# Optimization experiments

Measured on AMD Instinct MI355X. Metric: run time of the kernel, lower is better.

## Reference

```python
import jax, jax.numpy as jnp
import numpy as np

NUM_LEVELS = 16
LEVEL_DIM = 2
BASE_RES = 16
MAX_RES = 2048
HASHMAP_SIZE = 1 << 19
N_POINTS = 2000000

# Instant-NGP geometric progression of grid resolutions
_scale = np.exp2(np.log2(MAX_RES / BASE_RES) / (NUM_LEVELS - 1))
RESOLUTIONS = [int(np.ceil(BASE_RES * _scale ** l)) for l in range(NUM_LEVELS)]

# corner offsets of the unit cube, shape [8, 3]
_OFFS = np.stack(np.meshgrid([0, 1], [0, 1], [0, 1], indexing='ij'), -1).reshape(8, 3)
_PRIMES = np.array([1, 2654435761, 805459861], dtype=np.uint32)


def grid_encode(x, table):
    """x: [N,3] in [0,1]; table: [L, T, F] -> [N, L*F]."""
    offs = jnp.asarray(_OFFS, dtype=jnp.int32)          # [8,3]
    feats = []
    for l, res in enumerate(RESOLUTIONS):
        pos = x * (res - 1)                              # [N,3]
        pos_i = jnp.clip(jnp.floor(pos).astype(jnp.int32), 0, res - 2)
        frac = pos - pos_i.astype(pos.dtype)             # [N,3]
        corners = pos_i[:, None, :] + offs[None]         # [N,8,3]
        if res ** 3 <= HASHMAP_SIZE:
            # dense (collision-free) indexing for coarse levels
            idx = corners[..., 0] + res * (corners[..., 1] + res * corners[..., 2])
        else:
            # spatial hash: xor of coordinate * prime, mod table size
            c = corners.astype(jnp.uint32)
            h = (c[..., 0] * _PRIMES[0]) ^ (c[..., 1] * _PRIMES[1]) ^ (c[..., 2] * _PRIMES[2])
            idx = (h % jnp.uint32(HASHMAP_SIZE)).astype(jnp.int32)
        vals = table[l][idx]                             # [N,8,F] gather
        # multilinear interpolation weights per corner
        w = jnp.prod(jnp.where(offs[None].astype(bool), frac[:, None, :], 1.0 - frac[:, None, :]), axis=-1)  # [N,8]
        feats.append(jnp.einsum('nc,ncf->nf', w, vals))
    return jnp.concatenate(feats, axis=-1)               # [N, 32]


def setup_inputs() -> dict:
    key = jax.random.key(0)
    ks = jax.random.split(key, 6)
    x = jax.random.uniform(ks[0], (N_POINTS, 3), dtype=jnp.float32)
    table = jax.random.uniform(ks[1], (NUM_LEVELS, HASHMAP_SIZE, LEVEL_DIM),
                               dtype=jnp.float32, minval=-1e-4, maxval=1e-4)
    in_dim = NUM_LEVELS * LEVEL_DIM  # 32
    W1 = jax.random.normal(ks[2], (in_dim, 64), dtype=jnp.float32) / np.sqrt(in_dim)
    W2 = jax.random.normal(ks[3], (64, 64), dtype=jnp.float32) / 8.0
    W3 = jax.random.normal(ks[4], (64, 64), dtype=jnp.float32) / 8.0
    Wo = jax.random.normal(ks[5], (64, 1), dtype=jnp.float32) / 8.0
    z = lambda n: jnp.zeros((n,), dtype=jnp.float32)
    return {"x": x, "table": table, "W1": W1, "b1": z(64), "W2": W2, "b2": z(64),
            "W3": W3, "b3": z(64), "Wo": Wo, "bo": z(1)}


def reference(x, table, W1, b1, W2, b2, W3, b3, Wo, bo):
    h = grid_encode(x, table)                 # [N,32]
    h = jax.nn.relu(h @ W1 + b1)
    h = jax.nn.relu(h @ W2 + b2)
    h = jax.nn.relu(h @ W3 + b3)
    return h @ Wo + bo                        # [N,1]
```

## Files before the change

### kernel.cpp

```cpp
#include <hip/hip_runtime.h>
#include <cmath>
#include <cstdint>


#define HASH_SZ (1u << 19)
#define HMASK   (HASH_SZ - 1u)
#define PR2 2654435761u
#define PR3 805459861u

typedef float v2f __attribute__((ext_vector_type(2)));
typedef float v4f __attribute__((ext_vector_type(4)));
typedef v4f v4fu __attribute__((aligned(8)));
typedef v2f v2fu __attribute__((aligned(8)));
typedef short bf16x8 __attribute__((ext_vector_type(8)));
typedef float f32x4 __attribute__((ext_vector_type(4)));
typedef unsigned int u32;
typedef u32 u32x2 __attribute__((ext_vector_type(2)));
typedef u32 u32x4 __attribute__((ext_vector_type(4)));

struct ResArr { int r[16]; };

__device__ __forceinline__ unsigned short bf16_rne(float f) {
    union { float f; unsigned u; } v; v.f = f;
    unsigned u = v.u;
    unsigned r = (u + 0x7fffu + ((u >> 16) & 1u)) >> 16;
    return (unsigned short)r;
}
__device__ __forceinline__ float bf16f(unsigned short h) {
    union { unsigned u; float f; } v; v.u = ((unsigned)h) << 16;
    return v.f;
}
__device__ __forceinline__ void split8(const float* x, bf16x8& hi, bf16x8& lo) {
    #pragma unroll
    for (int j = 0; j < 8; ++j) {
        union { float f; unsigned u; } v; v.f = x[j];
        const unsigned hu = v.u & 0xffff0000u;
        hi[j] = (short)(hu >> 16);
        union { unsigned u; float f; } hf; hf.u = hu;
        const float d = x[j] - hf.f;
        union { float f; unsigned u; } dv; dv.f = d;
        lo[j] = (short)((dv.u + 0x7fffu + ((dv.u >> 16) & 1u)) >> 16);
    }
}
__device__ __forceinline__ u32 rne16u(float f) {
    union { float f; u32 u; } v; v.f = f;
    return (v.u + 0x7fffu + ((v.u >> 16) & 1u)) >> 16;
}
__device__ __forceinline__ u32x2 pack_split2(float f0, float f1) {
    union { float f; u32 u; } a, b; a.f = f0; b.f = f1;
    const u32 h0 = a.u & 0xffff0000u, h1 = b.u & 0xffff0000u;
    union { u32 u; float f; } ha, hb; ha.u = h0; hb.u = h1;
    u32x2 r;
    r.x = (h0 >> 16) | h1;
    r.y = rne16u(f0 - ha.f) | (rne16u(f1 - hb.f) << 16);
    return r;
}

__device__ __forceinline__ void gather_one(
    const v2f* __restrict__ tbl, int res, bool dense,
    float px, float py, float pz, float& A0, float& A1)
{
    const float rf = (float)(res - 1);
    const float fx = px * rf, fy = py * rf, fz = pz * rf;
    int ix = (int)floorf(fx), iy = (int)floorf(fy), iz = (int)floorf(fz);
    ix = min(max(ix, 0), res - 2);
    iy = min(max(iy, 0), res - 2);
    iz = min(max(iz, 0), res - 2);
    const float tx = fx - (float)ix, ty = fy - (float)iy, tz = fz - (float)iz;
    const float sx = 1.f - tx, sy = 1.f - ty, sz = 1.f - tz;
    float a0 = 0.f, a1 = 0.f;

    if (dense) {
        const int b0 = ix + res * (iy + res * iz);
        v4fu P[4];
        #pragma unroll
        for (int c = 0; c < 4; ++c) {
            const int dy = c >> 1, dz = c & 1;
            P[c] = *(const v4fu*)((const float*)tbl + 2 * (b0 + res * dy + res * res * dz));
        }
        #pragma unroll
        for (int c = 0; c < 4; ++c) {
            const int dy = c >> 1, dz = c & 1;
            const float wyz = (dy ? ty : sy) * (dz ? tz : sz);
            const float w0 = sx * wyz, w1 = tx * wyz;
            a0 = fmaf(w0, P[c].x, a0); a1 = fmaf(w0, P[c].y, a1);
            a0 = fmaf(w1, P[c].z, a0); a1 = fmaf(w1, P[c].w, a1);
        }
    } else {
        uint32_t i0[4], i1[4];
        v4f P[4];
        #pragma unroll
        for (int c = 0; c < 4; ++c) {
            const int dy = c >> 1, dz = c & 1;
            const uint32_t r = (uint32_t)(iy + dy) * PR2 ^ (uint32_t)(iz + dz) * PR3;
            i0[c] = ((uint32_t)ix ^ r) & HMASK;
            i1[c] = ((uint32_t)(ix + 1) ^ r) & HMASK;
            P[c] = *(const v4f*)((const float*)tbl + 2 * (i0[c] & ~1u));
        }
        const bool odd = (ix & 1);
        v2f O[4];
        if (odd) {
            #pragma unroll
            for (int c = 0; c < 4; ++c) O[c] = tbl[i1[c]];
        } else {
            #pragma unroll
            for (int c = 0; c < 4; ++c) { v2f z = {0.f, 0.f}; O[c] = z; }
        }
        #pragma unroll
        for (int c = 0; c < 4; ++c) {
            const int dy = c >> 1, dz = c & 1;
            const bool hi = (i0[c] & 1);
            v2f c0, e;
            c0.x = hi ? P[c].z : P[c].x;  c0.y = hi ? P[c].w : P[c].y;
            e.x  = hi ? P[c].x : P[c].z;  e.y  = hi ? P[c].y : P[c].w;
            const v2f c1 = odd ? O[c] : e;
            const float wyz = (dy ? ty : sy) * (dz ? tz : sz);
            const float w0 = sx * wyz, w1 = tx * wyz;
            a0 = fmaf(w0, c0.x, a0); a1 = fmaf(w0, c0.y, a1);
            a0 = fmaf(w1, c1.x, a0); a1 = fmaf(w1, c1.y, a1);
        }
    }
    A0 = a0; A1 = a1;
}

template<int NLEV>
__global__ __launch_bounds__(256, 8)
void encode_k(const float* __restrict__ x, const float* __restrict__ table,
              u32x2* __restrict__ featT, int n, int lb, ResArr rv)
{
    const int nth2 = gridDim.x * 512;
    for (int q = (blockIdx.x * 256 + threadIdx.x) * 2; q < n; q += nth2) {
        float p0x, p0y, p0z, p1x, p1y, p1z;
        const bool two = (q + 1 < n);
        if (two) {
            const v4fu a = __builtin_nontemporal_load((const v4fu*)(x + 3 * q));
            const v2f  b = __builtin_nontemporal_load((const v2fu*)(x + 3 * q + 4));
            p0x = a.x; p0y = a.y; p0z = a.z; p1x = a.w; p1y = b.x; p1z = b.y;
        } else {
            p0x = x[3 * q]; p0y = x[3 * q + 1]; p0z = x[3 * q + 2];
            p1x = p0x; p1y = p0y; p1z = p0z;
        }
        #pragma unroll
        for (int il = 0; il < NLEV; ++il) {
            const int l = lb + il;
            const int res = rv.r[l];
            const bool dense = ((long long)res * res * res <= (long long)HASH_SZ);
            const v2f* tbl = (const v2f*)table + (size_t)l * HASH_SZ;
            float a00, a01, a10, a11;
            gather_one(tbl, res, dense, p0x, p0y, p0z, a00, a01);
            gather_one(tbl, res, dense, p1x, p1y, p1z, a10, a11);
            if (two) {
                const u32x2 e0 = pack_split2(a00, a01);
                const u32x2 e1 = pack_split2(a10, a11);
                u32x4 st; st.x = e0.x; st.y = e0.y; st.z = e1.x; st.w = e1.y;
                __builtin_nontemporal_store(st, (u32x4*)&featT[(size_t)l * n + q]);
            } else {
                __builtin_nontemporal_store(pack_split2(a00, a01),
                                            &featT[(size_t)l * n + q]);
            }
        }
    }
}

__global__ void prep_weights(const float* __restrict__ W1,
                             const float* __restrict__ W2,
                             const float* __restrict__ W3,
                             unsigned short* __restrict__ wb)
{
    const int tid = threadIdx.x;
    const int nb = tid >> 6, lane = tid & 63;
    const int l15 = lane & 15, q = lane >> 4;
    #pragma unroll
    for (int j = 0; j < 8; ++j) {
        const float v = W1[(q * 8 + j) * 64 + nb * 16 + l15];
        const unsigned short h = bf16_rne(v);
        wb[(nb * 64 + lane) * 8 + j] = h;
        wb[2048 + (nb * 64 + lane) * 8 + j] = bf16_rne(v - bf16f(h));
    }
    #pragma unroll
    for (int kb = 0; kb < 2; ++kb) {
        #pragma unroll
        for (int j = 0; j < 8; ++j) {
            const int row = kb * 32 + q * 8 + j;
            const int idx = ((kb * 4 + nb) * 64 + lane) * 8 + j;
            float v = W2[row * 64 + nb * 16 + l15];
            unsigned short h = bf16_rne(v);
            wb[4096 + idx] = h;
            wb[8192 + idx] = bf16_rne(v - bf16f(h));
            v = W3[row * 64 + nb * 16 + l15];
            h = bf16_rne(v);
            wb[12288 + idx] = h;
            wb[16384 + idx] = bf16_rne(v - bf16f(h));
        }
    }
}

__global__ __launch_bounds__(256, 4)
void mlp_mfma(const u32x2* __restrict__ featT,
              const unsigned short* __restrict__ wb,
              const float* __restrict__ b1, const float* __restrict__ b2,
              const float* __restrict__ b3,
              const float* __restrict__ Wo, const float* __restrict__ bo,
              float* __restrict__ out, int n)
{
    const int wave = threadIdx.x >> 6;
    const int lane = threadIdx.x & 63;
    const int l15 = lane & 15, quad = lane >> 4;
    const int p0 = (blockIdx.x * 4 + wave) * 32;
    if (p0 >= n) return;

    bf16x8 bh[2], bl[2];
    #pragma unroll
    for (int t = 0; t < 2; ++t) {
        const int p = p0 + t * 16 + l15;
        const int pl = (p < n) ? p : (n - 1);
        u32x4 hw, lw;
        #pragma unroll
        for (int jj = 0; jj < 4; ++jj) {
            const u32x2 v = featT[(size_t)(quad * 4 + jj) * n + pl];
            hw[jj] = v.x; lw[jj] = v.y;
        }
        bh[t] = *(bf16x8*)&hw;
        bl[t] = *(bf16x8*)&lw;
    }

    f32x4 acc[2][4];
    #pragma unroll
    for (int nb = 0; nb < 4; ++nb) {
        const bf16x8 wh = *(const bf16x8*)(wb + (nb * 64 + lane) * 8);
        const bf16x8 wl = *(const bf16x8*)(wb + 2048 + (nb * 64 + lane) * 8);
        const f32x4 bv = *(const f32x4*)(b1 + nb * 16 + quad * 4);
        #pragma unroll
        for (int t = 0; t < 2; ++t) {
            f32x4 c = bv;
            c = __builtin_amdgcn_mfma_f32_16x16x32_bf16(wh, bl[t], c, 0, 0, 0);
            c = __builtin_amdgcn_mfma_f32_16x16x32_bf16(wl, bh[t], c, 0, 0, 0);
            c = __builtin_amdgcn_mfma_f32_16x16x32_bf16(wh, bh[t], c, 0, 0, 0);
            acc[t][nb] = c;
        }
    }

    #pragma unroll
    for (int layer = 0; layer < 2; ++layer) {
        bf16x8 nh[2][2], nl[2][2];
        #pragma unroll
        for (int t = 0; t < 2; ++t) {
            #pragma unroll
            for (int kb = 0; kb < 2; ++kb) {
                float v[8];
                #pragma unroll
                for (int rr = 0; rr < 4; ++rr) {
                    float xq = fmaxf(acc[t][2 * kb][rr],     0.f);
                    float yq = fmaxf(acc[t][2 * kb + 1][rr], 0.f);
                    asm("v_permlane32_swap_b32 %0, %1" : "+v"(xq), "+v"(yq));
                    asm("v_permlane16_swap_b32 %0, %1" : "+v"(xq), "+v"(yq));
                    v[rr]     = xq;
                    v[4 + rr] = yq;
                }
                split8(v, nh[t][kb], nl[t][kb]);
            }
        }
        const int base_h = layer ? 12288 : 4096;
        const int base_l = layer ? 16384 : 8192;
        const float* __restrict__ bias = layer ? b3 : b2;
        #pragma unroll
        for (int nb = 0; nb < 4; ++nb) {
            const f32x4 bv = *(const f32x4*)(bias + nb * 16 + quad * 4);
            f32x4 c[2];
            #pragma unroll
            for (int t = 0; t < 2; ++t) c[t] = bv;
            #pragma unroll
            for (int kb = 0; kb < 2; ++kb) {
                const int idx = ((kb * 4 + nb) * 64 + lane) * 8;
                const bf16x8 wh = *(const bf16x8*)(wb + base_h + idx);
                const bf16x8 wl = *(const bf16x8*)(wb + base_l + idx);
                #pragma unroll
                for (int t = 0; t < 2; ++t) {
                    c[t] = __builtin_amdgcn_mfma_f32_16x16x32_bf16(wh, nl[t][kb], c[t], 0, 0, 0);
                    c[t] = __builtin_amdgcn_mfma_f32_16x16x32_bf16(wl, nh[t][kb], c[t], 0, 0, 0);
                    c[t] = __builtin_amdgcn_mfma_f32_16x16x32_bf16(wh, nh[t][kb], c[t], 0, 0, 0);
                }
            }
            #pragma unroll
            for (int t = 0; t < 2; ++t) acc[t][nb] = c[t];
        }
    }

    float part[2];
    #pragma unroll
    for (int t = 0; t < 2; ++t) {
        float s = 0.f;
        #pragma unroll
        for (int nb = 0; nb < 4; ++nb) {
            const f32x4 wo4 = *(const f32x4*)(Wo + nb * 16 + quad * 4);
            #pragma unroll
            for (int r = 0; r < 4; ++r)
                s = fmaf(fmaxf(acc[t][nb][r], 0.f), wo4[r], s);
        }
        part[t] = s;
    }
    #pragma unroll
    for (int t = 0; t < 2; ++t) {
        part[t] += __shfl_xor(part[t], 16, 64);
        part[t] += __shfl_xor(part[t], 32, 64);
    }
    if (quad == 0) {
        const float b = bo[0];
        #pragma unroll
        for (int t = 0; t < 2; ++t) {
            const int po = p0 + t * 16 + l15;
            if (po < n) out[po] = part[t] + b;
        }
    }
}

__global__ __launch_bounds__(256, 3)
void mlp_forward(const u32x2* __restrict__ featT,
                 const float* __restrict__ W1, const float* __restrict__ b1,
                 const float* __restrict__ W2, const float* __restrict__ b2,
                 const float* __restrict__ W3, const float* __restrict__ b3,
                 const float* __restrict__ Wo, const float* __restrict__ bo,
                 float* __restrict__ out, int n)
{
    const int p = blockIdx.x * 256 + threadIdx.x;
    if (p >= n) return;
    const v2f z2 = {0.f, 0.f};
    v2f A[32], B[32];
    #pragma unroll
    for (int jq = 0; jq < 16; ++jq) {
        const v4f b = *(const v4f*)(b1 + 4 * jq);
        A[2 * jq] = b.xy; A[2 * jq + 1] = b.zw;
    }
    #pragma unroll
    for (int l = 0; l < 16; ++l) {
        const u32x2 e = __builtin_nontemporal_load(&featT[(size_t)l * n + p]);
        union { u32 u; float f; } h0, h1, l0, l1;
        h0.u = e.x << 16; h1.u = e.x & 0xffff0000u;
        l0.u = e.y << 16; l1.u = e.y & 0xffff0000u;
        v2f f; f.x = h0.f + l0.f; f.y = h1.f + l1.f;
        const v4f* w0 = (const v4f*)(W1 + (size_t)(2 * l) * 64);
        const v4f* w1 = (const v4f*)(W1 + (size_t)(2 * l + 1) * 64);
        const v2f hh0 = {f.x, f.x}, hh1 = {f.y, f.y};
        #pragma unroll
        for (int jq = 0; jq < 16; ++jq) {
            const v4f wa = w0[jq];
            A[2 * jq]     = __builtin_elementwise_fma(hh0, wa.xy, A[2 * jq]);
            A[2 * jq + 1] = __builtin_elementwise_fma(hh0, wa.zw, A[2 * jq + 1]);
        }
        #pragma unroll
        for (int jq = 0; jq < 16; ++jq) {
            const v4f wb2 = w1[jq];
            A[2 * jq]     = __builtin_elementwise_fma(hh1, wb2.xy, A[2 * jq]);
            A[2 * jq + 1] = __builtin_elementwise_fma(hh1, wb2.zw, A[2 * jq + 1]);
        }
    }
    #pragma unroll
    for (int j = 0; j < 32; ++j) A[j] = __builtin_elementwise_max(A[j], z2);
    #pragma unroll
    for (int jq = 0; jq < 16; ++jq) {
        const v4f b = *(const v4f*)(b2 + 4 * jq);
        B[2 * jq] = b.xy; B[2 * jq + 1] = b.zw;
    }
    #pragma unroll
    for (int k = 0; k < 64; ++k) {
        const float hv = A[k >> 1][k & 1];
        const v2f h = {hv, hv};
        const v4f* w = (const v4f*)(W2 + (size_t)k * 64);
        #pragma unroll
        for (int jq = 0; jq < 16; ++jq) {
            const v4f wa = w[jq];
            B[2 * jq]     = __builtin_elementwise_fma(h, wa.xy, B[2 * jq]);
            B[2 * jq + 1] = __builtin_elementwise_fma(h, wa.zw, B[2 * jq + 1]);
        }
    }
    #pragma unroll
    for (int j = 0; j < 32; ++j) B[j] = __builtin_elementwise_max(B[j], z2);
    #pragma unroll
    for (int jq = 0; jq < 16; ++jq) {
        const v4f b = *(const v4f*)(b3 + 4 * jq);
        A[2 * jq] = b.xy; A[2 * jq + 1] = b.zw;
    }
    #pragma unroll
    for (int k = 0; k < 64; ++k) {
        const float hv = B[k >> 1][k & 1];
        const v2f h = {hv, hv};
        const v4f* w = (const v4f*)(W3 + (size_t)k * 64);
        #pragma unroll
        for (int jq = 0; jq < 16; ++jq) {
            const v4f wa = w[jq];
            A[2 * jq]     = __builtin_elementwise_fma(h, wa.xy, A[2 * jq]);
            A[2 * jq + 1] = __builtin_elementwise_fma(h, wa.zw, A[2 * jq + 1]);
        }
    }
    v2f o2 = z2;
    #pragma unroll
    for (int jq = 0; jq < 16; ++jq) {
        const v4f wa = *(const v4f*)(Wo + 4 * jq);
        o2 = __builtin_elementwise_fma(__builtin_elementwise_max(A[2 * jq], z2),     wa.xy, o2);
        o2 = __builtin_elementwise_fma(__builtin_elementwise_max(A[2 * jq + 1], z2), wa.zw, o2);
    }
    out[p] = o2.x + o2.y + bo[0];
}

__global__ __launch_bounds__(256, 2)
void hashpinn_fused(const float* __restrict__ x,
                    const float* __restrict__ table,
                    const float* __restrict__ W1, const float* __restrict__ b1,
                    const float* __restrict__ W2, const float* __restrict__ b2,
                    const float* __restrict__ W3, const float* __restrict__ b3,
                    const float* __restrict__ Wo, const float* __restrict__ bo,
                    float* __restrict__ out, int n, ResArr rv)
{
    const int p = blockIdx.x * 256 + threadIdx.x;
    if (p >= n) return;
    const float px = x[3*p+0], py = x[3*p+1], pz = x[3*p+2];
    float feat[32];
    #pragma unroll
    for (int l = 0; l < 16; ++l) {
        const int res = rv.r[l];
        const float rf = (float)(res - 1);
        const float fx = px*rf, fy = py*rf, fz = pz*rf;
        int ix=(int)floorf(fx), iy=(int)floorf(fy), iz=(int)floorf(fz);
        ix=min(max(ix,0),res-2); iy=min(max(iy,0),res-2); iz=min(max(iz,0),res-2);
        const float tx=fx-(float)ix, ty=fy-(float)iy, tz=fz-(float)iz;
        const float sx=1.f-tx, sy=1.f-ty, sz=1.f-tz;
        const float2* tbl=(const float2*)table+(size_t)l*HASH_SZ;
        const bool dense=((long long)res*res*res<=(long long)HASH_SZ);
        float a0=0.f, a1=0.f;
        #pragma unroll
        for (int c=0;c<8;++c){
            const uint32_t cx=(uint32_t)(ix+((c>>2)&1));
            const uint32_t cy=(uint32_t)(iy+((c>>1)&1));
            const uint32_t cz=(uint32_t)(iz+(c&1));
            uint32_t idx = dense ? cx+(uint32_t)res*(cy+(uint32_t)res*cz)
                                 : ((cx*1u ^ cy*PR2 ^ cz*PR3)&HMASK);
            const float2 v=tbl[idx];
            const float w=(((c>>2)&1)?tx:sx)*(((c>>1)&1)?ty:sy)*((c&1)?tz:sz);
            a0=fmaf(w,v.x,a0); a1=fmaf(w,v.y,a1);
        }
        feat[2*l]=a0; feat[2*l+1]=a1;
    }
    float A[64], B[64];
    #pragma unroll
    for (int j=0;j<64;++j) A[j]=b1[j];
    #pragma unroll
    for (int k=0;k<32;++k){ const float h=feat[k];
        #pragma unroll
        for (int j=0;j<64;++j) A[j]=fmaf(h,W1[k*64+j],A[j]); }
    #pragma unroll 1
    for (int it=0;it<2;++it){
        const float* W = it?W3:W2; const float* bb = it?b3:b2;
        #pragma unroll
        for (int j=0;j<64;++j){ A[j]=fmaxf(A[j],0.f); B[j]=bb[j]; }
        #pragma unroll
        for (int k=0;k<64;++k){ const float h=A[k];
            #pragma unroll
            for (int j=0;j<64;++j) B[j]=fmaf(h,W[k*64+j],B[j]); }
        #pragma unroll
        for (int j=0;j<64;++j) A[j]=B[j];
    }
    float o=bo[0];
    #pragma unroll
    for (int j=0;j<64;++j) o=fmaf(fmaxf(A[j],0.f),Wo[j],o);
    out[p]=o;
}

static inline void launch_encode(int nlev, const float* x, const float* table,
                                 u32x2* featT, int n, int lb, const ResArr& rv,
                                 hipStream_t stream) {
    const dim3 g(4096), b(256);
    switch (nlev) {
        case 1: hipLaunchKernelGGL(encode_k<1>, g, b, 0, stream, x, table, featT, n, lb, rv); break;
        case 2: hipLaunchKernelGGL(encode_k<2>, g, b, 0, stream, x, table, featT, n, lb, rv); break;
        case 3: hipLaunchKernelGGL(encode_k<3>, g, b, 0, stream, x, table, featT, n, lb, rv); break;
        case 4: hipLaunchKernelGGL(encode_k<4>, g, b, 0, stream, x, table, featT, n, lb, rv); break;
        case 5: hipLaunchKernelGGL(encode_k<5>, g, b, 0, stream, x, table, featT, n, lb, rv); break;
        case 6: hipLaunchKernelGGL(encode_k<6>, g, b, 0, stream, x, table, featT, n, lb, rv); break;
        case 7: hipLaunchKernelGGL(encode_k<7>, g, b, 0, stream, x, table, featT, n, lb, rv); break;
        default: hipLaunchKernelGGL(encode_k<8>, g, b, 0, stream, x, table, featT, n, lb, rv); break;
    }
}

extern "C" void kernel_launch(void* const* d_in, const int* in_sizes, int n_in,
                              void* d_out, int out_size, void* d_ws, size_t ws_size,
                              hipStream_t stream) {
    const float* x     = (const float*)d_in[0];
    const float* table = (const float*)d_in[1];
    const float* W1    = (const float*)d_in[2];
    const float* b1    = (const float*)d_in[3];
    const float* W2    = (const float*)d_in[4];
    const float* b2    = (const float*)d_in[5];
    const float* W3    = (const float*)d_in[6];
    const float* b3    = (const float*)d_in[7];
    const float* Wo    = (const float*)d_in[8];
    const float* bo    = (const float*)d_in[9];
    float* out = (float*)d_out;

    const int n = in_sizes[0] / 3;

    ResArr rv;
    const double scale = std::exp2(std::log2(2048.0 / 16.0) / 15.0);
    for (int l = 0; l < 16; ++l)
        rv.r[l] = (int)std::ceil(16.0 * std::pow(scale, (double)l));

    int dense_end = 0;
    while (dense_end < 16) {
        long long r = rv.r[dense_end];
        if (r * r * r <= (long long)HASH_SZ) ++dense_end; else break;
    }
    if (dense_end > 8) dense_end = 8;

    const size_t feat_bytes = (size_t)n * 16 * sizeof(u32x2);
    const size_t wb_bytes = 20480 * sizeof(unsigned short);

    if (ws_size >= feat_bytes + wb_bytes) {
        u32x2* featT = (u32x2*)d_ws;
        unsigned short* wb = (unsigned short*)((char*)d_ws + feat_bytes);

        hipLaunchKernelGGL(prep_weights, dim3(1), dim3(256), 0, stream, W1, W2, W3, wb);

        if (dense_end > 0)
            launch_encode(dense_end, x, table, featT, n, 0, rv, stream);
        for (int l = dense_end; l < 16; ++l)
            launch_encode(1, x, table, featT, n, l, rv, stream);

        const int nblocks = (n + 127) / 128;
        hipLaunchKernelGGL(mlp_mfma, dim3(nblocks), dim3(256), 0, stream,
                           featT, wb, b1, b2, b3, Wo, bo, out, n);
    } else if (ws_size >= feat_bytes) {
        u32x2* featT = (u32x2*)d_ws;
        if (dense_end > 0)
            launch_encode(dense_end, x, table, featT, n, 0, rv, stream);
        for (int l = dense_end; l < 16; ++l)
            launch_encode(1, x, table, featT, n, l, rv, stream);
        hipLaunchKernelGGL(mlp_forward, dim3((n + 255) / 256), dim3(256), 0, stream,
                           featT, W1, b1, W2, b2, W3, b3, Wo, bo, out, n);
    } else {
        hipLaunchKernelGGL(hashpinn_fused, dim3((n + 255) / 256), dim3(256), 0, stream,
                           x, table, W1, b1, W2, b2, W3, b3, Wo, bo, out, n, rv);
    }
}
```

Baseline: 1.077 ms.

## Convert hash table to fp16 and gather packed half-precision entries

Adds a pre-pass that converts the fp32 feature table to packed fp16 pairs in workspace, and new encode kernels that gather from this half-size table. Hashed levels load aligned 16-byte groups of four entries and reuse them for the x+1 neighbour, issuing an extra load only when that neighbour falls in the next group. The aim is to halve gather bandwidth and cache footprint for the random lookups. The cost is an extra conversion pass over the table on every call and fp16 rounding of the table values, which may affect accuracy.

```diff
diff --git a/kernel.cpp b/kernel.cpp
--- a/kernel.cpp
+++ b/kernel.cpp
@@ -1,4 +1,5 @@
 #include <hip/hip_runtime.h>
+#include <hip/hip_fp16.h>
 #include <cmath>
 #include <cstdint>
 
@@ -17,6 +18,7 @@
 typedef unsigned int u32;
 typedef u32 u32x2 __attribute__((ext_vector_type(2)));
 typedef u32 u32x4 __attribute__((ext_vector_type(4)));
+typedef u32x4 u32x4u __attribute__((aligned(8)));
 
 struct ResArr { int r[16]; };
 
@@ -54,6 +56,141 @@
     r.x = (h0 >> 16) | h1;
     r.y = rne16u(f0 - ha.f) | (rne16u(f1 - hb.f) << 16);
     return r;
+}
+
+__device__ __forceinline__ u32 pkh(float f0, float f1) {
+    const __half h0 = __float2half_rn(f0), h1 = __float2half_rn(f1);
+    return (u32)__half_as_ushort(h0) | ((u32)__half_as_ushort(h1) << 16);
+}
+__device__ __forceinline__ v2f cvt2(u32 e) {
+    __half2 h;
+    *reinterpret_cast<u32*>(&h) = e;
+    v2f r; r.x = __low2float(h); r.y = __high2float(h);
+    return r;
+}
+__device__ __forceinline__ u32 sel4(u32x4 P, u32 k) {
+    const u32 a = (k & 1u) ? P.y : P.x;
+    const u32 b = (k & 1u) ? P.w : P.z;
+    return (k & 2u) ? b : a;
+}
+
+__global__ __launch_bounds__(256, 8)
+void cvt_table(const float* __restrict__ table, u32* __restrict__ tab16, int total)
+{
+    const int e0 = (blockIdx.x * 256 + threadIdx.x) * 4;
+    if (e0 >= total) return;
+    const v4f a = __builtin_nontemporal_load((const v4f*)(table + 2 * (size_t)e0));
+    const v4f b = __builtin_nontemporal_load((const v4f*)(table + 2 * (size_t)e0 + 4));
+    u32x4 o;
+    o.x = pkh(a.x, a.y); o.y = pkh(a.z, a.w);
+    o.z = pkh(b.x, b.y); o.w = pkh(b.z, b.w);
+    *(u32x4*)(tab16 + e0) = o;
+}
+
+__device__ __forceinline__ void gather16_one(
+    const u32* __restrict__ tab, int res, bool dense,
+    float px, float py, float pz, float& A0, float& A1)
+{
+    const float rf = (float)(res - 1);
+    const float fx = px * rf, fy = py * rf, fz = pz * rf;
+    int ix = (int)floorf(fx), iy = (int)floorf(fy), iz = (int)floorf(fz);
+    ix = min(max(ix, 0), res - 2);
+    iy = min(max(iy, 0), res - 2);
+    iz = min(max(iz, 0), res - 2);
+    const float tx = fx - (float)ix, ty = fy - (float)iy, tz = fz - (float)iz;
+    const float sx = 1.f - tx, sy = 1.f - ty, sz = 1.f - tz;
+    float a0 = 0.f, a1 = 0.f;
+
+    if (dense) {
+        const int b0 = ix + res * (iy + res * iz);
+        #pragma unroll
+        for (int c = 0; c < 4; ++c) {
+            const int dy = c >> 1, dz = c & 1;
+            const u32 idx0 = (u32)(b0 + res * dy + res * res * dz);
+            const u32x4u Pv = *(const u32x4u*)(tab + (idx0 & ~1u));
+            const bool hi = (idx0 & 1u) != 0u;
+            const u32 e0 = hi ? Pv.y : Pv.x;
+            const u32 e1 = hi ? Pv.z : Pv.y;
+            const float wyz = (dy ? ty : sy) * (dz ? tz : sz);
+            const float w0 = sx * wyz, w1 = tx * wyz;
+            const v2f f0 = cvt2(e0), f1 = cvt2(e1);
+            a0 = fmaf(w0, f0.x, a0); a1 = fmaf(w0, f0.y, a1);
+            a0 = fmaf(w1, f1.x, a0); a1 = fmaf(w1, f1.y, a1);
+        }
+    } else {
+        u32 i1a[4], k0[4];
+        u32x4 P[4];
+        #pragma unroll
+        for (int c = 0; c < 4; ++c) {
+            const int dy = c >> 1, dz = c & 1;
+            const u32 r = (u32)(iy + dy) * PR2 ^ (u32)(iz + dz) * PR3;
+            const u32 i0 = ((u32)ix ^ r) & HMASK;
+            i1a[c] = ((u32)(ix + 1) ^ r) & HMASK;
+            k0[c] = i0 & 3u;
+            P[c] = *(const u32x4*)(tab + (i0 & ~3u));
+        }
+        const bool extra = ((ix & 3) == 3);
+        u32 O[4];
+        if (extra) {
+            #pragma unroll
+            for (int c = 0; c < 4; ++c) O[c] = tab[i1a[c]];
+        } else {
+            #pragma unroll
+            for (int c = 0; c < 4; ++c) O[c] = 0u;
+        }
+        #pragma unroll
+        for (int c = 0; c < 4; ++c) {
+            const int dy = c >> 1, dz = c & 1;
+            const u32 e0 = sel4(P[c], k0[c]);
+            const u32 e1w = sel4(P[c], i1a[c] & 3u);
+            const u32 e1 = extra ? O[c] : e1w;
+            const float wyz = (dy ? ty : sy) * (dz ? tz : sz);
+            const float w0 = sx * wyz, w1 = tx * wyz;
+            const v2f f0 = cvt2(e0), f1 = cvt2(e1);
+            a0 = fmaf(w0, f0.x, a0); a1 = fmaf(w0, f0.y, a1);
+            a0 = fmaf(w1, f1.x, a0); a1 = fmaf(w1, f1.y, a1);
+        }
+    }
+    A0 = a0; A1 = a1;
+}
+
+template<int NLEV>
+__global__ __launch_bounds__(256, 8)
+void encode16_k(const float* __restrict__ x, const u32* __restrict__ tab16,
+                u32x2* __restrict__ featT, int n, int lb, ResArr rv)
+{
+    const int nth2 = gridDim.x * 512;
+    for (int q = (blockIdx.x * 256 + threadIdx.x) * 2; q < n; q += nth2) {
+        float p0x, p0y, p0z, p1x, p1y, p1z;
+        const bool two = (q + 1 < n);
+        if (two) {
+            const v4fu a = __builtin_nontemporal_load((const v4fu*)(x + 3 * q));
+            const v2f  b = __builtin_nontemporal_load((const v2fu*)(x + 3 * q + 4));
+            p0x = a.x; p0y = a.y; p0z = a.z; p1x = a.w; p1y = b.x; p1z = b.y;
+        } else {
+            p0x = x[3 * q]; p0y = x[3 * q + 1]; p0z = x[3 * q + 2];
+            p1x = p0x; p1y = p0y; p1z = p0z;
+        }
+        #pragma unroll
+        for (int il = 0; il < NLEV; ++il) {
+            const int l = lb + il;
+            const int res = rv.r[l];
+            const bool dense = ((long long)res * res * res <= (long long)HASH_SZ);
+            const u32* tbl = tab16 + (size_t)l * HASH_SZ;
+            float a00, a01, a10, a11;
+            gather16_one(tbl, res, dense, p0x, p0y, p0z, a00, a01);
+            gather16_one(tbl, res, dense, p1x, p1y, p1z, a10, a11);
+            if (two) {
+                const u32x2 e0 = pack_split2(a00, a01);
+                const u32x2 e1 = pack_split2(a10, a11);
+                u32x4 st; st.x = e0.x; st.y = e0.y; st.z = e1.x; st.w = e1.y;
+                __builtin_nontemporal_store(st, (u32x4*)&featT[(size_t)l * n + q]);
+            } else {
+                __builtin_nontemporal_store(pack_split2(a00, a01),
+                                            &featT[(size_t)l * n + q]);
+            }
+        }
+    }
 }
 
 __device__ __forceinline__ void gather_one(
@@ -465,6 +602,22 @@
     out[p]=o;
 }
 
+static inline void launch_encode16(int nlev, const float* x, const u32* tab16,
+                                   u32x2* featT, int n, int lb, const ResArr& rv,
+                                   hipStream_t stream) {
+    const dim3 g(4096), b(256);
+    switch (nlev) {
+        case 1: hipLaunchKernelGGL(encode16_k<1>, g, b, 0, stream, x, tab16, featT, n, lb, rv); break;
+        case 2: hipLaunchKernelGGL(encode16_k<2>, g, b, 0, stream, x, tab16, featT, n, lb, rv); break;
+        case 3: hipLaunchKernelGGL(encode16_k<3>, g, b, 0, stream, x, tab16, featT, n, lb, rv); break;
+        case 4: hipLaunchKernelGGL(encode16_k<4>, g, b, 0, stream, x, tab16, featT, n, lb, rv); break;
+        case 5: hipLaunchKernelGGL(encode16_k<5>, g, b, 0, stream, x, tab16, featT, n, lb, rv); break;
+        case 6: hipLaunchKernelGGL(encode16_k<6>, g, b, 0, stream, x, tab16, featT, n, lb, rv); break;
+        case 7: hipLaunchKernelGGL(encode16_k<7>, g, b, 0, stream, x, tab16, featT, n, lb, rv); break;
+        default: hipLaunchKernelGGL(encode16_k<8>, g, b, 0, stream, x, tab16, featT, n, lb, rv); break;
+    }
+}
+
 static inline void launch_encode(int nlev, const float* x, const float* table,
                                  u32x2* featT, int n, int lb, const ResArr& rv,
                                  hipStream_t stream) {
@@ -512,8 +665,27 @@
 
     const size_t feat_bytes = (size_t)n * 16 * sizeof(u32x2);
     const size_t wb_bytes = 20480 * sizeof(unsigned short);
-
-    if (ws_size >= feat_bytes + wb_bytes) {
+    const size_t tab16_bytes = (size_t)16 * HASH_SZ * sizeof(u32);
+    const int total_entries = 16 * (int)HASH_SZ;
+
+    if (ws_size >= feat_bytes + wb_bytes + tab16_bytes) {
+        u32x2* featT = (u32x2*)d_ws;
+        unsigned short* wb = (unsigned short*)((char*)d_ws + feat_bytes);
+        u32* tab16 = (u32*)((char*)d_ws + feat_bytes + wb_bytes);
+
+        hipLaunchKernelGGL(prep_weights, dim3(1), dim3(256), 0, stream, W1, W2, W3, wb);
+        hipLaunchKernelGGL(cvt_table, dim3(8192), dim3(256), 0, stream,
+                           table, tab16, total_entries);
+
+        if (dense_end > 0)
+            launch_encode16(dense_end, x, tab16, featT, n, 0, rv, stream);
+        for (int l = dense_end; l < 16; ++l)
+            launch_encode16(1, x, tab16, featT, n, l, rv, stream);
+
+        const int nblocks = (n + 127) / 128;
+        hipLaunchKernelGGL(mlp_mfma, dim3(nblocks), dim3(256), 0, stream,
+                           featT, wb, b1, b2, b3, Wo, bo, out, n);
+    } else if (ws_size >= feat_bytes + wb_bytes) {
         u32x2* featT = (u32x2*)d_ws;
         unsigned short* wb = (unsigned short*)((char*)d_ws + feat_bytes);
 
```

New measurement: 1.077 ms. No clear change (-0.1%).
